# Performance work log

Measured on AMD Instinct MI355X. Metric: run time of the kernel, lower is better.

## Reference

```python
import jax, jax.numpy as jnp
import numpy as np

EPS = 1e-8        # LinearGELU eps
LN_EPS = 1e-5     # LayerNorm eps
NUM_HEADS = 16
DIM = 1024
HIDDEN = 4096
B, N = 4, 785


def _lin(x, xj, w, lw, b=None, lb=None):
    # LinearLinear: primal linear + JVP wrt input and tangent params (lw, lb)
    y = x @ w.T
    yj = xj @ w.T + x @ lw.T
    if b is not None:
        y = y + b
    if lb is not None:
        yj = yj + lb
    return y, yj


def _ln(x, xj, w, b, lw, lb):
    # LinearLayerNorm forward + manual JVP (matches torch source exactly)
    mean = x.mean(-1, keepdims=True)
    xc = x - mean
    var = (xc * xc).mean(-1, keepdims=True)
    std = jnp.sqrt(var + LN_EPS)
    xhat = xc / std
    out = xhat * w + b
    t1 = xhat * lw + lb                              # tangent wrt affine params
    mj = xj.mean(-1, keepdims=True)
    xjc = xj - mj
    a = xjc * std
    corr = 2.0 * (xc * xjc).mean(-1, keepdims=True)
    bterm = (0.5 / std) * corr * xc
    c = (1.0 / std) ** 2 * (a - bterm)
    return out, t1 + c * w


def _gelu(x, xj):
    # exact (erf) GELU; jvp uses gelu(x)/(x+EPS) + x*pdf(x) as in source
    out = 0.5 * x * (1.0 + jax.lax.erf(x * np.float32(1.0 / np.sqrt(2.0))))
    pdf = jnp.exp(-0.5 * x * x) * np.float32(1.0 / np.sqrt(2.0 * np.pi))
    return out, xj * (out / (x + EPS) + x * pdf)


def _attn(x, xj, qkv_w, qkv_lw, proj_w, proj_b, proj_lw, proj_lb):
    Bb, Nn, C = x.shape
    H = NUM_HEADS
    D = C // H
    scale = np.float32(D) ** -0.5
    qkv, qkv_j = _lin(x, xj, qkv_w, qkv_lw)  # [B,N,3C], qkv_bias=False
    def split(t):
        return t.reshape(Bb, Nn, 3, H, D).transpose(2, 0, 3, 1, 4)
    q, k, v = split(qkv)
    qj, kj, vj = split(qkv_j)
    q = q * scale
    qj = qj * scale
    attn = jax.nn.softmax(jnp.einsum('bhnd,bhmd->bhnm', q, k), axis=-1)
    out = jnp.einsum('bhnm,bhmd->bhnd', attn, v)
    # softmax JVP: dm = A_jvp + B_jvp; filter = dm*attn - rowsum(dm*attn)*attn
    dm = jnp.einsum('bhnd,bhmd->bhnm', qj, k) + jnp.einsum('bhnd,bhmd->bhnm', q, kj)
    f = dm * attn
    filt = f - f.sum(-1, keepdims=True) * attn  # == diag(dm @ attn^T) * attn correction
    out_j = jnp.einsum('bhnm,bhmd->bhnd', filt, v) + jnp.einsum('bhnm,bhmd->bhnd', attn, vj)
    out = out.transpose(0, 2, 1, 3).reshape(Bb, Nn, C)
    out_j = out_j.transpose(0, 2, 1, 3).reshape(Bb, Nn, C)
    return _lin(out, out_j, proj_w, proj_lw, proj_b, proj_lb)


def setup_inputs() -> dict:
    keys = jax.random.split(jax.random.key(0), 32)
    ki = iter(keys)
    def nrm(shape, s=0.02):
        return (jax.random.normal(next(ki), shape, jnp.float32) * s).astype(jnp.float32)
    d, h = DIM, HIDDEN
    inp = {
        'input': jax.random.normal(next(ki), (B, N, d), jnp.float32),
        'input_jvp': jax.random.normal(next(ki), (B, N, d), jnp.float32),
        'n1_w': 1.0 + nrm((d,), 0.1), 'n1_b': nrm((d,), 0.1),
        'n1_lw': nrm((d,), 0.1), 'n1_lb': nrm((d,), 0.1),
        'qkv_w': nrm((3 * d, d)), 'qkv_lw': nrm((3 * d, d)),
        'proj_w': nrm((d, d)), 'proj_b': nrm((d,), 0.1),
        'proj_lw': nrm((d, d)), 'proj_lb': nrm((d,), 0.1),
        'n2_w': 1.0 + nrm((d,), 0.1), 'n2_b': nrm((d,), 0.1),
        'n2_lw': nrm((d,), 0.1), 'n2_lb': nrm((d,), 0.1),
        'fc1_w': nrm((h, d)), 'fc1_b': nrm((h,), 0.1),
        'fc1_lw': nrm((h, d)), 'fc1_lb': nrm((h,), 0.1),
        'fc2_w': nrm((d, h)), 'fc2_b': nrm((d,), 0.1),
        'fc2_lw': nrm((d, h)), 'fc2_lb': nrm((d,), 0.1),
    }
    return inp


def reference(input, input_jvp, n1_w, n1_b, n1_lw, n1_lb, qkv_w, qkv_lw,
              proj_w, proj_b, proj_lw, proj_lb, n2_w, n2_b, n2_lw, n2_lb,
              fc1_w, fc1_b, fc1_lw, fc1_lb, fc2_w, fc2_b, fc2_lw, fc2_lb):
    x, xj = _ln(input, input_jvp, n1_w, n1_b, n1_lw, n1_lb)
    x, xj = _attn(x, xj, qkv_w, qkv_lw, proj_w, proj_b, proj_lw, proj_lb)
    x = x + input
    xj = xj + input_jvp
    i2, i2j = x, xj
    x, xj = _ln(x, xj, n2_w, n2_b, n2_lw, n2_lb)
    x, xj = _lin(x, xj, fc1_w, fc1_lw, fc1_b, fc1_lb)
    x, xj = _gelu(x, xj)
    x, xj = _lin(x, xj, fc2_w, fc2_lw, fc2_b, fc2_lb)
    return (x + i2, xj + i2j)
```

## Files before the change

### kernel.cpp

```cpp
#include <hip/hip_runtime.h>
#include <hip/hip_bf16.h>

typedef unsigned short u16;
typedef unsigned int   u32;

#define MP     3328
#define MREAL  3140
#define DIMC   1024
#define H3C    3072
#define HIDC   4096
#define NKV    785
#define SLEN   896

typedef __bf16 bf16x8 __attribute__((ext_vector_type(8)));
typedef float  f32x4  __attribute__((ext_vector_type(4)));

#define MFMA(d,a,b) (d) = __builtin_amdgcn_mfma_f32_16x16x32_bf16((a),(b),(d),0,0,0)

__device__ __forceinline__ u16 f2bf(float f){
  u32 u = __builtin_bit_cast(u32, f);
  return (u16)((u + 0x7fffu + ((u >> 16) & 1u)) >> 16);
}
__device__ __forceinline__ float bf2f(u16 h){
  return __builtin_bit_cast(float, (u32)h << 16);
}
__device__ __forceinline__ void gload16(const u16* g, u16* l){
  __builtin_amdgcn_global_load_lds(
      (const __attribute__((address_space(1))) void*)g,
      (__attribute__((address_space(3))) void*)l, 16, 0, 0);
}
__device__ __forceinline__ float wsum(float v){
  #pragma unroll
  for (int o = 32; o >= 1; o >>= 1) v += __shfl_xor(v, o);
  return v;
}

__global__ __launch_bounds__(256) void cvt_k(const float* __restrict__ in,
                                             u16* __restrict__ out, int n){
  int i = (blockIdx.x * 256 + threadIdx.x) * 4;
  if (i >= n) return;
  float4 v = *(const float4*)(in + i);
  ushort4 o4;
  o4.x = f2bf(v.x); o4.y = f2bf(v.y); o4.z = f2bf(v.z); o4.w = f2bf(v.w);
  *(ushort4*)(out + i) = o4;
}

__global__ __launch_bounds__(256) void ln_jvp_k(
    const float* __restrict__ x, const float* __restrict__ xj,
    const float* __restrict__ w, const float* __restrict__ b,
    const float* __restrict__ lw, const float* __restrict__ lb,
    u16* __restrict__ out, u16* __restrict__ outj)
{
  const int row = blockIdx.x, t = threadIdx.x;
  const size_t ro = (size_t)row * DIMC;
  if (row >= MREAL){
    for (int i = t; i < DIMC; i += 256){ out[ro+i] = 0; outj[ro+i] = 0; }
    return;
  }
  const float4 v  = ((const float4*)(x  + ro))[t];
  const float4 vj = ((const float4*)(xj + ro))[t];
  float sx  = v.x+v.y+v.z+v.w;
  float sxx = v.x*v.x+v.y*v.y+v.z*v.z+v.w*v.w;
  float sj  = vj.x+vj.y+vj.z+vj.w;
  float sxj = v.x*vj.x+v.y*vj.y+v.z*vj.z+v.w*vj.w;
  __shared__ __attribute__((aligned(64))) float red[4][4];
  sx = wsum(sx); sxx = wsum(sxx); sj = wsum(sj); sxj = wsum(sxj);
  const int wid = t>>6, lane = t&63;
  if (lane == 0){ red[wid][0]=sx; red[wid][1]=sxx; red[wid][2]=sj; red[wid][3]=sxj; }
  __syncthreads();
  sx  = red[0][0]+red[1][0]+red[2][0]+red[3][0];
  sxx = red[0][1]+red[1][1]+red[2][1]+red[3][1];
  sj  = red[0][2]+red[1][2]+red[2][2]+red[3][2];
  sxj = red[0][3]+red[1][3]+red[2][3]+red[3][3];
  const float inv  = 1.0f/1024.0f;
  const float mean = sx*inv, meanj = sj*inv;
  const float var  = sxx*inv - mean*mean;
  const float cov  = sxj*inv - mean*meanj;
  const float rstd = rsqrtf(var + 1e-5f);
  const float r3   = rstd*rstd*rstd;
  const float4 wv  = ((const float4*)w)[t];
  const float4 bv  = ((const float4*)b)[t];
  const float4 lwv = ((const float4*)lw)[t];
  const float4 lbv = ((const float4*)lb)[t];
  const float xs[4]  = {v.x,v.y,v.z,v.w},   xjs[4] = {vj.x,vj.y,vj.z,vj.w};
  const float wss[4] = {wv.x,wv.y,wv.z,wv.w}, bs[4] = {bv.x,bv.y,bv.z,bv.w};
  const float lws[4] = {lwv.x,lwv.y,lwv.z,lwv.w}, lbs[4] = {lbv.x,lbv.y,lbv.z,lbv.w};
  const int i0 = t*4;
  #pragma unroll
  for (int e = 0; e < 4; e++){
    const float xc = xs[e]-mean, xjc = xjs[e]-meanj;
    const float xhat = xc*rstd;
    const float cc = xjc*rstd - xc*cov*r3;
    out [ro+i0+e] = f2bf(xhat*wss[e] + bs[e]);
    outj[ro+i0+e] = f2bf(xhat*lws[e] + lbs[e] + cc*wss[e]);
  }
}

template<int EPI>
__global__ __launch_bounds__(512, 1) void gemm_jvp_wide_k(
    const u16* __restrict__ A, const u16* __restrict__ Aj, int lda,
    const u16* __restrict__ B, const u16* __restrict__ Bj, int K,
    const float* __restrict__ bias, const float* __restrict__ biasj,
    void* __restrict__ Yv, void* __restrict__ Yjv, int ldy)
{
  __shared__ __attribute__((aligned(128))) u16 lds[3][24576];
  const int tid = threadIdx.x, wid = tid>>6, lane = tid&63;
  const int l4 = lane>>4, l15 = lane&15;
  const int m0 = blockIdx.y*256, n0 = blockIdx.x*128;
  f32x4 accY[4][4], accJ[4][4];
  #pragma unroll
  for (int i = 0; i < 4; i++)
    #pragma unroll
    for (int j = 0; j < 4; j++){
      accY[i][j] = (f32x4){0.f,0.f,0.f,0.f};
      accJ[i][j] = (f32x4){0.f,0.f,0.f,0.f};
    }
  const int boA0 = tid*16,        boA1 = (512+tid)*16;
  const int sbA0 = boA0 ^ (((boA0>>7)&7)<<4);
  const int sbA1 = boA1 ^ (((boA1>>7)&7)<<4);
  const int rA0 = sbA0>>6, cA0 = (sbA0&63)>>1;
  const int rA1 = sbA1>>6, cA1 = (sbA1&63)>>1;
  const int boB = tid*16;
  const int sbB = boB ^ (((boB>>7)&7)<<4);
  const int rB = sbB>>6, cB = (sbB&63)>>1;
  const u16* srcA0  = A  + (size_t)(m0+rA0)*lda + cA0;
  const u16* srcA1  = A  + (size_t)(m0+rA1)*lda + cA1;
  const u16* srcAj0 = Aj + (size_t)(m0+rA0)*lda + cA0;
  const u16* srcAj1 = Aj + (size_t)(m0+rA1)*lda + cA1;
  const u16* srcB   = B  + (size_t)(n0+rB)*K + cB;
  const u16* srcBj  = Bj + (size_t)(n0+rB)*K + cB;
  const int dA0 = tid*8, dA1 = (512+tid)*8, dB = tid*8;
  const int wr = wid>>1, wc = wid&1;
  int aoff[4], boff[4];
  #pragma unroll
  for (int i = 0; i < 4; i++){
    int ab_ = (wr*64 + i*16 + l15)*64 + l4*16;
    aoff[i] = ab_ ^ (((ab_>>7)&7)<<4);
    int bb_ = (wc*64 + i*16 + l15)*64 + l4*16;
    boff[i] = bb_ ^ (((bb_>>7)&7)<<4);
  }
  auto STAGE = [&](int buf, int t){
    const int k0 = t<<5;
    u16* Lb = &lds[buf][0];
    gload16(srcA0 +k0, Lb + dA0);
    gload16(srcA1 +k0, Lb + dA1);
    gload16(srcAj0+k0, Lb + 8192 + dA0);
    gload16(srcAj1+k0, Lb + 8192 + dA1);
    gload16(srcB  +k0, Lb + 16384 + dB);
    gload16(srcBj +k0, Lb + 20480 + dB);
  };
  const int nt = K >> 5;
  STAGE(0, 0);
  STAGE(1, 1);
  for (int t = 0; t < nt; t++){
    if (t + 1 < nt) asm volatile("s_waitcnt vmcnt(6)" ::: "memory");
    else            asm volatile("s_waitcnt vmcnt(0)" ::: "memory");
    __builtin_amdgcn_s_barrier();
    if (t + 2 < nt) STAGE((t+2)%3, t+2);
    const char* Lb = (const char*)&lds[t%3][0];
    bf16x8 af[4], ajf[4], bbf[4], bjf[4];
    #pragma unroll
    for (int i = 0; i < 4; i++){
      af[i]  = *(const bf16x8*)(Lb + aoff[i]);
      ajf[i] = *(const bf16x8*)(Lb + 16384 + aoff[i]);
      bbf[i] = *(const bf16x8*)(Lb + 32768 + boff[i]);
      bjf[i] = *(const bf16x8*)(Lb + 40960 + boff[i]);
    }
    __builtin_amdgcn_s_setprio(1);
    #pragma unroll
    for (int i = 0; i < 4; i++)
      #pragma unroll
      for (int j = 0; j < 4; j++){
        MFMA(accY[i][j], af[i],  bbf[j]);
        MFMA(accJ[i][j], ajf[i], bbf[j]);
        MFMA(accJ[i][j], af[i],  bjf[j]);
      }
    __builtin_amdgcn_s_setprio(0);
  }
  const int mb = m0 + wr*64 + (l4<<2);
  const int nb = n0 + wc*64 + l15;
  #pragma unroll
  for (int i = 0; i < 4; i++)
    #pragma unroll
    for (int j = 0; j < 4; j++)
      #pragma unroll
      for (int r = 0; r < 4; r++){
        const int m = mb + i*16 + r, n = nb + j*16;
        float y = accY[i][j][r], yj = accJ[i][j][r];
        if (EPI == 0){
          ((u16*)Yv )[(size_t)m*ldy+n] = f2bf(y);
          ((u16*)Yjv)[(size_t)m*ldy+n] = f2bf(yj);
        } else {
          y  += bias[n];
          yj += biasj[n];
          const float ge  = 0.5f*y*(1.0f + erff(y*0.70710678118654752f));
          const float pdf = __expf(-0.5f*y*y)*0.3989422804014327f;
          const float gj  = yj*(ge/(y + 1e-8f) + y*pdf);
          ((u16*)Yv )[(size_t)m*ldy+n] = f2bf(ge);
          ((u16*)Yjv)[(size_t)m*ldy+n] = f2bf(gj);
        }
      }
}

template<int EPI>
__global__ __launch_bounds__(256) void gemm_jvp_k(
    const u16* __restrict__ A, const u16* __restrict__ Aj, int lda,
    const u16* __restrict__ B, const u16* __restrict__ Bj, int K,
    const float* __restrict__ bias, const float* __restrict__ biasj,
    const float* __restrict__ res, const float* __restrict__ resj,
    void* __restrict__ Yv, void* __restrict__ Yjv, int ldy, int mwrite)
{
  __shared__ __attribute__((aligned(128))) u16 lds[3][4][128*32];
  const int tid = threadIdx.x, wid = tid>>6, lane = tid&63;
  const int m0 = blockIdx.y*128, n0 = blockIdx.x*128;
  f32x4 accY[4][4], accJ[4][4];
  #pragma unroll
  for (int i = 0; i < 4; i++)
    #pragma unroll
    for (int j = 0; j < 4; j++){
      accY[i][j] = (f32x4){0.f,0.f,0.f,0.f};
      accJ[i][j] = (f32x4){0.f,0.f,0.f,0.f};
    }
  const int bo0 = wid*1024 + lane*16;
  const int bo1 = bo0 + 4096;
  const int sb0 = bo0 ^ (((bo0>>7)&7)<<4);
  const int sb1 = bo1 ^ (((bo1>>7)&7)<<4);
  const int r0 = sb0>>6, c0 = (sb0&63)>>1;
  const int r1 = sb1>>6, c1 = (sb1&63)>>1;
  const u16* A0  = A  + (size_t)(m0+r0)*lda + c0;
  const u16* A1  = A  + (size_t)(m0+r1)*lda + c1;
  const u16* Aj0 = Aj + (size_t)(m0+r0)*lda + c0;
  const u16* Aj1 = Aj + (size_t)(m0+r1)*lda + c1;
  const u16* B0  = B  + (size_t)(n0+r0)*K + c0;
  const u16* B1  = B  + (size_t)(n0+r1)*K + c1;
  const u16* Bj0 = Bj + (size_t)(n0+r0)*K + c0;
  const u16* Bj1 = Bj + (size_t)(n0+r1)*K + c1;
  const int kq = (lane>>4)<<3;
  const int ar = (wid>>1)*64 + (lane&15);
  const int bc = (wid&1)*64 + (lane&15);
  int aoff[4], boff[4];
  #pragma unroll
  for (int i = 0; i < 4; i++){
    int ab_ = (ar+i*16)*64 + (kq<<1);
    aoff[i] = ab_ ^ (((ab_>>7)&7)<<4);
    int bb_ = (bc+i*16)*64 + (kq<<1);
    boff[i] = bb_ ^ (((bb_>>7)&7)<<4);
  }
  auto STAGE = [&](int buf, int t){
    const int k0 = t<<5;
    u16* p0 = &lds[buf][0][0];
    gload16(A0 +k0, p0+(bo0>>1)); gload16(A1 +k0, p0+(bo1>>1));
    u16* p1 = &lds[buf][1][0];
    gload16(Aj0+k0, p1+(bo0>>1)); gload16(Aj1+k0, p1+(bo1>>1));
    u16* p2 = &lds[buf][2][0];
    gload16(B0 +k0, p2+(bo0>>1)); gload16(B1 +k0, p2+(bo1>>1));
    u16* p3 = &lds[buf][3][0];
    gload16(Bj0+k0, p3+(bo0>>1)); gload16(Bj1+k0, p3+(bo1>>1));
  };
  const int nt = K >> 5;
  STAGE(0, 0);
  STAGE(1, 1);
  for (int t = 0; t < nt; t++){
    if (t + 1 < nt) asm volatile("s_waitcnt vmcnt(8)" ::: "memory");
    else            asm volatile("s_waitcnt vmcnt(0)" ::: "memory");
    __builtin_amdgcn_s_barrier();
    if (t + 2 < nt) STAGE((t+2)%3, t+2);
    const char* lAb  = (const char*)&lds[t%3][0][0];
    const char* lAjb = (const char*)&lds[t%3][1][0];
    const char* lBb  = (const char*)&lds[t%3][2][0];
    const char* lBjb = (const char*)&lds[t%3][3][0];
    bf16x8 af[4], ajf[4], bbf[4], bjf[4];
    #pragma unroll
    for (int i = 0; i < 4; i++){
      af[i]  = *(const bf16x8*)(lAb  + aoff[i]);
      ajf[i] = *(const bf16x8*)(lAjb + aoff[i]);
      bbf[i] = *(const bf16x8*)(lBb  + boff[i]);
      bjf[i] = *(const bf16x8*)(lBjb + boff[i]);
    }
    __builtin_amdgcn_s_setprio(1);
    #pragma unroll
    for (int i = 0; i < 4; i++)
      #pragma unroll
      for (int j = 0; j < 4; j++){
        MFMA(accY[i][j], af[i],  bbf[j]);
        MFMA(accJ[i][j], ajf[i], bbf[j]);
        MFMA(accJ[i][j], af[i],  bjf[j]);
      }
    __builtin_amdgcn_s_setprio(0);
  }
  const int mb = m0 + (wid>>1)*64 + ((lane>>4)<<2);
  const int nb = n0 + (wid&1)*64 + (lane&15);
  #pragma unroll
  for (int i = 0; i < 4; i++)
    #pragma unroll
    for (int j = 0; j < 4; j++)
      #pragma unroll
      for (int r = 0; r < 4; r++){
        const int m = mb + i*16 + r, n = nb + j*16;
        float y = accY[i][j][r], yj = accJ[i][j][r];
        if (EPI == 0){
          ((u16*)Yv )[(size_t)m*ldy+n] = f2bf(y);
          ((u16*)Yjv)[(size_t)m*ldy+n] = f2bf(yj);
        } else if (EPI == 1){
          if (m < mwrite){
            y  += bias[n]  + res [(size_t)m*ldy+n];
            yj += biasj[n] + resj[(size_t)m*ldy+n];
            ((float*)Yv )[(size_t)m*ldy+n] = y;
            ((float*)Yjv)[(size_t)m*ldy+n] = yj;
          }
        } else {
          y  += bias[n];
          yj += biasj[n];
          const float ge  = 0.5f*y*(1.0f + erff(y*0.70710678118654752f));
          const float pdf = __expf(-0.5f*y*y)*0.3989422804014327f;
          const float gj  = yj*(ge/(y + 1e-8f) + y*pdf);
          ((u16*)Yv )[(size_t)m*ldy+n] = f2bf(ge);
          ((u16*)Yjv)[(size_t)m*ldy+n] = f2bf(gj);
        }
      }
}

__global__ __launch_bounds__(256) void transpose_v_k(
    const u16* __restrict__ qkvb, const u16* __restrict__ qkvjb,
    u16* __restrict__ vT, u16* __restrict__ vjT)
{
  __shared__ __attribute__((aligned(64))) u16 tl[64][80];
  __shared__ __attribute__((aligned(64))) u16 tlj[64][80];
  const int kt = blockIdx.x, bh = blockIdx.y;
  const int b = bh>>4, h = bh&15;
  const int t = threadIdx.x;
  const int kv = t>>2, dd = (t&3)*16;
  const int kvg = kt*64 + kv;
  if (kvg < NKV){
    const u16* s0 = qkvb  + (size_t)(b*NKV+kvg)*H3C + 2048 + h*64 + dd;
    const u16* s1 = qkvjb + (size_t)(b*NKV+kvg)*H3C + 2048 + h*64 + dd;
    *(uint4*)&tl [kv][dd]   = *(const uint4*)s0;
    *(uint4*)&tl [kv][dd+8] = *(const uint4*)(s0+8);
    *(uint4*)&tlj[kv][dd]   = *(const uint4*)s1;
    *(uint4*)&tlj[kv][dd+8] = *(const uint4*)(s1+8);
  } else {
    uint4 z = {0,0,0,0};
    *(uint4*)&tl [kv][dd] = z; *(uint4*)&tl [kv][dd+8] = z;
    *(uint4*)&tlj[kv][dd] = z; *(uint4*)&tlj[kv][dd+8] = z;
  }
  __syncthreads();
  const int d = t>>2, kc = (t&3)*16;
  u16* d0 = vT  + ((size_t)bh*64 + d)*SLEN + kt*64 + kc;
  u16* d1 = vjT + ((size_t)bh*64 + d)*SLEN + kt*64 + kc;
  #pragma unroll
  for (int e = 0; e < 16; e++){ d0[e] = tl[kc+e][d]; d1[e] = tlj[kc+e][d]; }
}

__global__ __launch_bounds__(256) void flash_attn_jvp_k(
    const u16* __restrict__ qkvb, const u16* __restrict__ qkvjb,
    const u16* __restrict__ vT, const u16* __restrict__ vjT,
    u16* __restrict__ o, u16* __restrict__ oj)
{
  __shared__ __attribute__((aligned(64))) u16 lK  [64*64];
  __shared__ __attribute__((aligned(64))) u16 lKj [64*64];
  __shared__ __attribute__((aligned(64))) u16 lvT [64*64];
  __shared__ __attribute__((aligned(64))) u16 lvjT[64*64];
  __shared__ __attribute__((aligned(64))) u16 pl  [128*64];
  __shared__ __attribute__((aligned(64))) u16 pdl [128*64];
  const int tid = threadIdx.x, wid = tid>>6, lane = tid&63;
  const int l4 = lane>>4, l15 = lane&15;
  const int qt = blockIdx.x, bh = blockIdx.y, b = bh>>4, h = bh&15;

  bf16x8 qf[2][2], qjf[2][2];
  {
    const size_t qrb = (size_t)b*NKV + qt*128 + wid*32;
    #pragma unroll
    for (int i = 0; i < 2; i++){
      const size_t ro = (qrb + i*16 + l15)*H3C + h*64;
      #pragma unroll
      for (int ks = 0; ks < 2; ks++){
        qf [i][ks] = *(const bf16x8*)(qkvb  + ro + ks*32 + l4*8);
        qjf[i][ks] = *(const bf16x8*)(qkvjb + ro + ks*32 + l4*8);
      }
    }
  }
  float m_st[2][4], l_st[2][4], g_st[2][4];
  f32x4 PO[2][4], PTJ[2][4];
  #pragma unroll
  for (int i = 0; i < 2; i++)
    #pragma unroll
    for (int r = 0; r < 4; r++){
      m_st[i][r] = -1e30f; l_st[i][r] = 0.f; g_st[i][r] = 0.f;
    }
  #pragma unroll
  for (int i = 0; i < 2; i++)
    #pragma unroll
    for (int j = 0; j < 4; j++){
      PO[i][j] = (f32x4){0.f,0.f,0.f,0.f};
      PTJ[i][j] = (f32x4){0.f,0.f,0.f,0.f};
    }
  const char* lKb   = (const char*)lK;
  const char* lKjb  = (const char*)lKj;
  const char* lvTb  = (const char*)lvT;
  const char* lvjTb = (const char*)lvjT;
  char* plb  = (char*)pl;
  char* pdlb = (char*)pdl;

  for (int t = 0; t < 13; t++){
    #pragma unroll
    for (int rnd = 0; rnd < 2; rnd++){
      const int gidx = rnd*256 + tid;
      const int row = gidx>>3, c = gidx&7;
      const int cs = c ^ (row&7);
      const size_t ksrc = (size_t)(b*NKV + t*64 + row)*H3C + 1024 + h*64 + cs*8;
      gload16(qkvb  + ksrc, lK  + gidx*8);
      gload16(qkvjb + ksrc, lKj + gidx*8);
      const size_t vsrc = ((size_t)bh*64 + row)*SLEN + t*64 + cs*8;
      gload16(vT  + vsrc, lvT  + gidx*8);
      gload16(vjT + vsrc, lvjT + gidx*8);
    }
    __syncthreads();

    #pragma unroll
    for (int i = 0; i < 2; i++){
      f32x4 s[4], dm[4];
      #pragma unroll
      for (int j = 0; j < 4; j++){
        s[j] = (f32x4){0.f,0.f,0.f,0.f};
        dm[j] = (f32x4){0.f,0.f,0.f,0.f};
      }
      #pragma unroll
      for (int ks = 0; ks < 2; ks++){
        #pragma unroll
        for (int j = 0; j < 4; j++){
          const int row = j*16 + l15;
          const int byt = (row*128 + ks*64 + l4*16) ^ ((row&7)<<4);
          const bf16x8 kf  = *(const bf16x8*)(lKb  + byt);
          const bf16x8 kjf = *(const bf16x8*)(lKjb + byt);
          MFMA(s[j],  qf[i][ks],  kf);
          MFMA(dm[j], qjf[i][ks], kf);
          MFMA(dm[j], qf[i][ks],  kjf);
        }
      }
      float tm[4] = {-1e30f,-1e30f,-1e30f,-1e30f};
      #pragma unroll
      for (int j = 0; j < 4; j++){
        const int colg = t*64 + j*16 + l15;
        #pragma unroll
        for (int r = 0; r < 4; r++){
          float sv = s[j][r]*0.125f;
          if (colg >= NKV) sv = -1e30f;
          s[j][r] = sv;
          dm[j][r] *= 0.125f;
          tm[r] = fmaxf(tm[r], sv);
        }
      }
      #pragma unroll
      for (int r = 0; r < 4; r++){
        float v = tm[r];
        v = fmaxf(v, __shfl_xor(v, 1));
        v = fmaxf(v, __shfl_xor(v, 2));
        v = fmaxf(v, __shfl_xor(v, 4));
        v = fmaxf(v, __shfl_xor(v, 8));
        const float mn = fmaxf(m_st[i][r], v);
        const float sc = __expf(m_st[i][r] - mn);
        m_st[i][r] = mn;
        l_st[i][r] *= sc;
        g_st[i][r] *= sc;
        #pragma unroll
        for (int j = 0; j < 4; j++){ PO[i][j][r] *= sc; PTJ[i][j][r] *= sc; }
      }
      float ps[4] = {0.f,0.f,0.f,0.f}, pds[4] = {0.f,0.f,0.f,0.f};
      #pragma unroll
      for (int j = 0; j < 4; j++){
        const int col = j*16 + l15;
        #pragma unroll
        for (int r = 0; r < 4; r++){
          const float p  = __expf(s[j][r] - m_st[i][r]);
          const float pd = p * dm[j][r];
          ps[r] += p; pds[r] += pd;
          const int row = wid*32 + i*16 + l4*4 + r;
          const int byt = (row*128 + col*2) ^ ((row&7)<<4);
          *(u16*)(plb  + byt) = f2bf(p);
          *(u16*)(pdlb + byt) = f2bf(pd);
        }
      }
      #pragma unroll
      for (int r = 0; r < 4; r++){
        float v = ps[r], w = pds[r];
        v += __shfl_xor(v, 1); w += __shfl_xor(w, 1);
        v += __shfl_xor(v, 2); w += __shfl_xor(w, 2);
        v += __shfl_xor(v, 4); w += __shfl_xor(w, 4);
        v += __shfl_xor(v, 8); w += __shfl_xor(w, 8);
        l_st[i][r] += v; g_st[i][r] += w;
      }
    }

    #pragma unroll
    for (int ks = 0; ks < 2; ks++){
      bf16x8 pa[2], pda[2];
      #pragma unroll
      for (int i = 0; i < 2; i++){
        const int row = wid*32 + i*16 + l15;
        const int byt = (row*128 + ks*64 + l4*16) ^ ((row&7)<<4);
        pa[i]  = *(const bf16x8*)(plb  + byt);
        pda[i] = *(const bf16x8*)(pdlb + byt);
      }
      #pragma unroll
      for (int j = 0; j < 4; j++){
        const int row = j*16 + l15;
        const int byt = (row*128 + ks*64 + l4*16) ^ ((row&7)<<4);
        const bf16x8 vb  = *(const bf16x8*)(lvTb  + byt);
        const bf16x8 vjb = *(const bf16x8*)(lvjTb + byt);
        #pragma unroll
        for (int i = 0; i < 2; i++){
          MFMA(PO[i][j],  pa[i],  vb);
          MFMA(PTJ[i][j], pda[i], vb);
          MFMA(PTJ[i][j], pa[i],  vjb);
        }
      }
    }
    __syncthreads();
  }

  #pragma unroll
  for (int i = 0; i < 2; i++)
    #pragma unroll
    for (int r = 0; r < 4; r++){
      const int ql = qt*128 + wid*32 + i*16 + l4*4 + r;
      if (ql < NKV){
        const float rl = 1.0f / l_st[i][r];
        const float gg = g_st[i][r] * rl;
        #pragma unroll
        for (int j = 0; j < 4; j++){
          const size_t oo = ((size_t)b*NKV + ql)*DIMC + h*64 + j*16 + l15;
          const float po = PO[i][j][r] * rl;
          o [oo] = f2bf(po);
          oj[oo] = f2bf(PTJ[i][j][r]*rl - gg*po);
        }
      }
    }
}

extern "C" void kernel_launch(void* const* d_in, const int* in_sizes, int n_in,
                              void* d_out, int out_size, void* d_ws, size_t ws_size,
                              hipStream_t stream)
{
  (void)in_sizes; (void)n_in; (void)out_size;
  const float* input   = (const float*)d_in[0];
  const float* inputj  = (const float*)d_in[1];
  const float* n1_w    = (const float*)d_in[2];
  const float* n1_b    = (const float*)d_in[3];
  const float* n1_lw   = (const float*)d_in[4];
  const float* n1_lb   = (const float*)d_in[5];
  const float* qkv_w   = (const float*)d_in[6];
  const float* qkv_lw  = (const float*)d_in[7];
  const float* proj_w  = (const float*)d_in[8];
  const float* proj_b  = (const float*)d_in[9];
  const float* proj_lw = (const float*)d_in[10];
  const float* proj_lb = (const float*)d_in[11];
  const float* n2_w    = (const float*)d_in[12];
  const float* n2_b    = (const float*)d_in[13];
  const float* n2_lw   = (const float*)d_in[14];
  const float* n2_lb   = (const float*)d_in[15];
  const float* fc1_w   = (const float*)d_in[16];
  const float* fc1_b   = (const float*)d_in[17];
  const float* fc1_lw  = (const float*)d_in[18];
  const float* fc1_lb  = (const float*)d_in[19];
  const float* fc2_w   = (const float*)d_in[20];
  const float* fc2_b   = (const float*)d_in[21];
  const float* fc2_lw  = (const float*)d_in[22];
  const float* fc2_lb  = (const float*)d_in[23];

  const size_t SZ_W      = 2u*4194304u*2u;
  const size_t SZ_ARENA1 = 2u*(size_t)MP*HIDC*2u;
  const size_t SZ_VT     = (size_t)64*64*SLEN*2u;
  const size_t SZ_ARENA2 = 2u*SZ_VT;
  const size_t SZ_ARENA3 = 2u*(size_t)MP*DIMC*2u;
  const size_t SZ_X2     = (size_t)MP*DIMC*4u;
  const size_t NEEDED = SZ_W + SZ_ARENA1 + SZ_ARENA2 + SZ_ARENA3 + 2u*SZ_X2 + 4096u;
  if (ws_size < NEEDED) return;

  char* base = (char*)d_ws;
  size_t off = 0;
  auto ab = [&](size_t bytes)->char*{
    char* p = base + off;
    off += bytes; off = (off + 255) & ~(size_t)255;
    return p;
  };
  char* Wslot  = ab(SZ_W);
  char* arena1 = ab(SZ_ARENA1);
  char* arena2 = ab(SZ_ARENA2);
  char* arena3 = ab(SZ_ARENA3);
  float* x2  = (float*)ab(SZ_X2);
  float* x2j = (float*)ab(SZ_X2);

  u16* wbuf  = (u16*)Wslot;
  u16* wjbuf = wbuf + 4194304;
  u16* qkvb  = (u16*)arena1;
  u16* qkvjb = qkvb + (size_t)MP*H3C;
  u16* hb    = (u16*)arena1;
  u16* hjb   = hb + (size_t)MP*HIDC;
  u16* vT    = (u16*)arena2;
  u16* vjT   = vT + (size_t)64*64*SLEN;
  u16* x3b   = (u16*)arena2;
  u16* x3jb  = x3b + (size_t)MP*DIMC;
  u16* x1b   = (u16*)arena3;
  u16* x1jb  = x1b + (size_t)MP*DIMC;
  u16* ob    = (u16*)arena3;
  u16* ojb   = ob + (size_t)MP*DIMC;

  auto cvt = [&](const float* src, u16* dst, int n){
    cvt_k<<<dim3((n + 1023)/1024), 256, 0, stream>>>(src, dst, n);
  };

  ln_jvp_k<<<dim3(MP), 256, 0, stream>>>(input, inputj, n1_w, n1_b, n1_lw, n1_lb,
                                         x1b, x1jb);
  cvt(qkv_w, wbuf, H3C*DIMC); cvt(qkv_lw, wjbuf, H3C*DIMC);
  gemm_jvp_wide_k<0><<<dim3(H3C/128, MP/256), 512, 0, stream>>>(
      x1b, x1jb, DIMC, wbuf, wjbuf, DIMC, nullptr, nullptr,
      qkvb, qkvjb, H3C);
  transpose_v_k<<<dim3(14, 64), 256, 0, stream>>>(qkvb, qkvjb, vT, vjT);
  flash_attn_jvp_k<<<dim3(7, 64), 256, 0, stream>>>(qkvb, qkvjb, vT, vjT, ob, ojb);
  cvt(proj_w, wbuf, DIMC*DIMC); cvt(proj_lw, wjbuf, DIMC*DIMC);
  gemm_jvp_k<1><<<dim3(DIMC/128, MP/128), 256, 0, stream>>>(
      ob, ojb, DIMC, wbuf, wjbuf, DIMC, proj_b, proj_lb, input, inputj,
      x2, x2j, DIMC, MREAL);
  ln_jvp_k<<<dim3(MP), 256, 0, stream>>>(x2, x2j, n2_w, n2_b, n2_lw, n2_lb,
                                         x3b, x3jb);
  cvt(fc1_w, wbuf, HIDC*DIMC); cvt(fc1_lw, wjbuf, HIDC*DIMC);
  gemm_jvp_wide_k<2><<<dim3(HIDC/128, MP/256), 512, 0, stream>>>(
      x3b, x3jb, DIMC, wbuf, wjbuf, DIMC, fc1_b, fc1_lb,
      hb, hjb, HIDC);
  cvt(fc2_w, wbuf, DIMC*HIDC); cvt(fc2_lw, wjbuf, DIMC*HIDC);
  float* out0 = (float*)d_out;
  float* out1 = out0 + (size_t)MREAL*DIMC;
  gemm_jvp_k<1><<<dim3(DIMC/128, MP/128), 256, 0, stream>>>(
      hb, hjb, HIDC, wbuf, wjbuf, HIDC, fc2_b, fc2_lb, x2, x2j,
      out0, out1, DIMC, MREAL);
}
```

Baseline: 557.2 us.

## Retile wide JVP GEMM to 128x256 with 4 waves, XCD-aware block remap, fused cvt

The wide GEMM used for QKV and FC1 changes from 512 threads with 256x128 tiles to 256 threads with 128x256 tiles. Each wave now holds a 64x128 output with 4x8 accumulator pairs, so every A fragment loaded from LDS is reused across twice as many MFMAs. Both GEMM kernels remap block indices round-robin over 8 chiplets so that neighbouring tiles land on the same XCD and share L2. The two weight-conversion launches per layer are merged into one kernel. The costs are much higher register pressure (256 fp32 accumulator values per lane) and fewer, larger blocks per GEMM.

```diff
diff --git a/kernel.cpp b/kernel.cpp
--- a/kernel.cpp
+++ b/kernel.cpp
@@ -35,14 +35,18 @@
   return v;
 }
 
-__global__ __launch_bounds__(256) void cvt_k(const float* __restrict__ in,
-                                             u16* __restrict__ out, int n){
+__global__ __launch_bounds__(256) void cvt2_k(
+    const float* __restrict__ in0, u16* __restrict__ out0, int n0,
+    const float* __restrict__ in1, u16* __restrict__ out1, int n1)
+{
   int i = (blockIdx.x * 256 + threadIdx.x) * 4;
-  if (i >= n) return;
-  float4 v = *(const float4*)(in + i);
+  const float* src; u16* dst;
+  if (i < n0){ src = in0 + i; dst = out0 + i; }
+  else { int j = i - n0; if (j >= n1) return; src = in1 + j; dst = out1 + j; }
+  float4 v = *(const float4*)src;
   ushort4 o4;
   o4.x = f2bf(v.x); o4.y = f2bf(v.y); o4.z = f2bf(v.z); o4.w = f2bf(v.w);
-  *(ushort4*)(out + i) = o4;
+  *(ushort4*)dst = o4;
 }
 
 __global__ __launch_bounds__(256) void ln_jvp_k(
@@ -97,7 +101,7 @@
 }
 
 template<int EPI>
-__global__ __launch_bounds__(512, 1) void gemm_jvp_wide_k(
+__global__ __launch_bounds__(256, 1) void gemm_jvp_v2_k(
     const u16* __restrict__ A, const u16* __restrict__ Aj, int lda,
     const u16* __restrict__ B, const u16* __restrict__ Bj, int K,
     const float* __restrict__ bias, const float* __restrict__ biasj,
@@ -106,71 +110,96 @@
   __shared__ __attribute__((aligned(128))) u16 lds[3][24576];
   const int tid = threadIdx.x, wid = tid>>6, lane = tid&63;
   const int l4 = lane>>4, l15 = lane&15;
-  const int m0 = blockIdx.y*256, n0 = blockIdx.x*128;
-  f32x4 accY[4][4], accJ[4][4];
+  const int ord = blockIdx.y * gridDim.x + blockIdx.x;
+  const int cpx = (gridDim.x * gridDim.y) >> 3;
+  const int nb  = (ord & 7) * cpx + (ord >> 3);
+  const int m0 = (nb / gridDim.x) * 128;
+  const int n0 = (nb % gridDim.x) * 256;
+  f32x4 accY[4][8], accJ[4][8];
   #pragma unroll
   for (int i = 0; i < 4; i++)
     #pragma unroll
-    for (int j = 0; j < 4; j++){
+    for (int j = 0; j < 8; j++){
       accY[i][j] = (f32x4){0.f,0.f,0.f,0.f};
       accJ[i][j] = (f32x4){0.f,0.f,0.f,0.f};
     }
-  const int boA0 = tid*16,        boA1 = (512+tid)*16;
-  const int sbA0 = boA0 ^ (((boA0>>7)&7)<<4);
-  const int sbA1 = boA1 ^ (((boA1>>7)&7)<<4);
-  const int rA0 = sbA0>>6, cA0 = (sbA0&63)>>1;
-  const int rA1 = sbA1>>6, cA1 = (sbA1&63)>>1;
-  const int boB = tid*16;
-  const int sbB = boB ^ (((boB>>7)&7)<<4);
-  const int rB = sbB>>6, cB = (sbB&63)>>1;
+  const int bA0 = tid*16,        bA1 = (256+tid)*16;
+  const int sA0 = bA0 ^ (((bA0>>7)&7)<<4), sA1 = bA1 ^ (((bA1>>7)&7)<<4);
+  const int rA0 = sA0>>6, cA0 = (sA0&63)>>1;
+  const int rA1 = sA1>>6, cA1 = (sA1&63)>>1;
+  int rB[4], cB[4];
+  #pragma unroll
+  for (int g = 0; g < 4; g++){
+    const int bb = (g*256 + tid)*16;
+    const int sb = bb ^ (((bb>>7)&7)<<4);
+    rB[g] = sb>>6; cB[g] = (sb&63)>>1;
+  }
   const u16* srcA0  = A  + (size_t)(m0+rA0)*lda + cA0;
   const u16* srcA1  = A  + (size_t)(m0+rA1)*lda + cA1;
   const u16* srcAj0 = Aj + (size_t)(m0+rA0)*lda + cA0;
   const u16* srcAj1 = Aj + (size_t)(m0+rA1)*lda + cA1;
-  const u16* srcB   = B  + (size_t)(n0+rB)*K + cB;
-  const u16* srcBj  = Bj + (size_t)(n0+rB)*K + cB;
-  const int dA0 = tid*8, dA1 = (512+tid)*8, dB = tid*8;
+  const u16* srcB0  = B  + (size_t)(n0+rB[0])*K + cB[0];
+  const u16* srcB1  = B  + (size_t)(n0+rB[1])*K + cB[1];
+  const u16* srcB2  = B  + (size_t)(n0+rB[2])*K + cB[2];
+  const u16* srcB3  = B  + (size_t)(n0+rB[3])*K + cB[3];
+  const u16* srcBj0 = Bj + (size_t)(n0+rB[0])*K + cB[0];
+  const u16* srcBj1 = Bj + (size_t)(n0+rB[1])*K + cB[1];
+  const u16* srcBj2 = Bj + (size_t)(n0+rB[2])*K + cB[2];
+  const u16* srcBj3 = Bj + (size_t)(n0+rB[3])*K + cB[3];
+  const int dA0 = tid*8, dA1 = (256+tid)*8;
   const int wr = wid>>1, wc = wid&1;
-  int aoff[4], boff[4];
+  int aoff[4], boff[8];
   #pragma unroll
   for (int i = 0; i < 4; i++){
     int ab_ = (wr*64 + i*16 + l15)*64 + l4*16;
     aoff[i] = ab_ ^ (((ab_>>7)&7)<<4);
-    int bb_ = (wc*64 + i*16 + l15)*64 + l4*16;
-    boff[i] = bb_ ^ (((bb_>>7)&7)<<4);
+  }
+  #pragma unroll
+  for (int j = 0; j < 8; j++){
+    int bb_ = (wc*128 + j*16 + l15)*64 + l4*16;
+    boff[j] = bb_ ^ (((bb_>>7)&7)<<4);
   }
   auto STAGE = [&](int buf, int t){
     const int k0 = t<<5;
     u16* Lb = &lds[buf][0];
     gload16(srcA0 +k0, Lb + dA0);
     gload16(srcA1 +k0, Lb + dA1);
-    gload16(srcAj0+k0, Lb + 8192 + dA0);
-    gload16(srcAj1+k0, Lb + 8192 + dA1);
-    gload16(srcB  +k0, Lb + 16384 + dB);
-    gload16(srcBj +k0, Lb + 20480 + dB);
+    gload16(srcAj0+k0, Lb + 4096 + dA0);
+    gload16(srcAj1+k0, Lb + 4096 + dA1);
+    gload16(srcB0 +k0, Lb + 8192  + tid*8);
+    gload16(srcB1 +k0, Lb + 8192  + (256+tid)*8);
+    gload16(srcB2 +k0, Lb + 8192  + (512+tid)*8);
+    gload16(srcB3 +k0, Lb + 8192  + (768+tid)*8);
+    gload16(srcBj0+k0, Lb + 16384 + tid*8);
+    gload16(srcBj1+k0, Lb + 16384 + (256+tid)*8);
+    gload16(srcBj2+k0, Lb + 16384 + (512+tid)*8);
+    gload16(srcBj3+k0, Lb + 16384 + (768+tid)*8);
   };
   const int nt = K >> 5;
   STAGE(0, 0);
   STAGE(1, 1);
   for (int t = 0; t < nt; t++){
-    if (t + 1 < nt) asm volatile("s_waitcnt vmcnt(6)" ::: "memory");
+    if (t + 1 < nt) asm volatile("s_waitcnt vmcnt(12)" ::: "memory");
     else            asm volatile("s_waitcnt vmcnt(0)" ::: "memory");
     __builtin_amdgcn_s_barrier();
     if (t + 2 < nt) STAGE((t+2)%3, t+2);
     const char* Lb = (const char*)&lds[t%3][0];
-    bf16x8 af[4], ajf[4], bbf[4], bjf[4];
+    bf16x8 af[4], ajf[4], bbf[8], bjf[8];
     #pragma unroll
     for (int i = 0; i < 4; i++){
       af[i]  = *(const bf16x8*)(Lb + aoff[i]);
-      ajf[i] = *(const bf16x8*)(Lb + 16384 + aoff[i]);
-      bbf[i] = *(const bf16x8*)(Lb + 32768 + boff[i]);
-      bjf[i] = *(const bf16x8*)(Lb + 40960 + boff[i]);
+      ajf[i] = *(const bf16x8*)(Lb + 8192 + aoff[i]);
+    }
+    #pragma unroll
+    for (int j = 0; j < 8; j++){
+      bbf[j] = *(const bf16x8*)(Lb + 16384 + boff[j]);
+      bjf[j] = *(const bf16x8*)(Lb + 32768 + boff[j]);
     }
     __builtin_amdgcn_s_setprio(1);
     #pragma unroll
     for (int i = 0; i < 4; i++)
       #pragma unroll
-      for (int j = 0; j < 4; j++){
+      for (int j = 0; j < 8; j++){
         MFMA(accY[i][j], af[i],  bbf[j]);
         MFMA(accJ[i][j], ajf[i], bbf[j]);
         MFMA(accJ[i][j], af[i],  bjf[j]);
@@ -178,14 +207,14 @@
     __builtin_amdgcn_s_setprio(0);
   }
   const int mb = m0 + wr*64 + (l4<<2);
-  const int nb = n0 + wc*64 + l15;
+  const int nbase = n0 + wc*128 + l15;
   #pragma unroll
   for (int i = 0; i < 4; i++)
     #pragma unroll
-    for (int j = 0; j < 4; j++)
+    for (int j = 0; j < 8; j++)
       #pragma unroll
       for (int r = 0; r < 4; r++){
-        const int m = mb + i*16 + r, n = nb + j*16;
+        const int m = mb + i*16 + r, n = nbase + j*16;
         float y = accY[i][j][r], yj = accJ[i][j][r];
         if (EPI == 0){
           ((u16*)Yv )[(size_t)m*ldy+n] = f2bf(y);
@@ -212,7 +241,11 @@
 {
   __shared__ __attribute__((aligned(128))) u16 lds[3][4][128*32];
   const int tid = threadIdx.x, wid = tid>>6, lane = tid&63;
-  const int m0 = blockIdx.y*128, n0 = blockIdx.x*128;
+  const int ord = blockIdx.y * gridDim.x + blockIdx.x;
+  const int cpx = (gridDim.x * gridDim.y) >> 3;
+  const int nbk = (ord & 7) * cpx + (ord >> 3);
+  const int m0 = (nbk / gridDim.x) * 128;
+  const int n0 = (nbk % gridDim.x) * 128;
   f32x4 accY[4][4], accJ[4][4];
   #pragma unroll
   for (int i = 0; i < 4; i++)
@@ -605,29 +638,30 @@
   u16* ob    = (u16*)arena3;
   u16* ojb   = ob + (size_t)MP*DIMC;
 
-  auto cvt = [&](const float* src, u16* dst, int n){
-    cvt_k<<<dim3((n + 1023)/1024), 256, 0, stream>>>(src, dst, n);
+  auto cvt2 = [&](const float* s0, u16* d0, int n0,
+                  const float* s1, u16* d1, int n1){
+    cvt2_k<<<dim3((n0 + n1 + 1023)/1024), 256, 0, stream>>>(s0, d0, n0, s1, d1, n1);
   };
 
   ln_jvp_k<<<dim3(MP), 256, 0, stream>>>(input, inputj, n1_w, n1_b, n1_lw, n1_lb,
                                          x1b, x1jb);
-  cvt(qkv_w, wbuf, H3C*DIMC); cvt(qkv_lw, wjbuf, H3C*DIMC);
-  gemm_jvp_wide_k<0><<<dim3(H3C/128, MP/256), 512, 0, stream>>>(
+  cvt2(qkv_w, wbuf, H3C*DIMC, qkv_lw, wjbuf, H3C*DIMC);
+  gemm_jvp_v2_k<0><<<dim3(H3C/256, MP/128), 256, 0, stream>>>(
       x1b, x1jb, DIMC, wbuf, wjbuf, DIMC, nullptr, nullptr,
       qkvb, qkvjb, H3C);
   transpose_v_k<<<dim3(14, 64), 256, 0, stream>>>(qkvb, qkvjb, vT, vjT);
   flash_attn_jvp_k<<<dim3(7, 64), 256, 0, stream>>>(qkvb, qkvjb, vT, vjT, ob, ojb);
-  cvt(proj_w, wbuf, DIMC*DIMC); cvt(proj_lw, wjbuf, DIMC*DIMC);
+  cvt2(proj_w, wbuf, DIMC*DIMC, proj_lw, wjbuf, DIMC*DIMC);
   gemm_jvp_k<1><<<dim3(DIMC/128, MP/128), 256, 0, stream>>>(
       ob, ojb, DIMC, wbuf, wjbuf, DIMC, proj_b, proj_lb, input, inputj,
       x2, x2j, DIMC, MREAL);
   ln_jvp_k<<<dim3(MP), 256, 0, stream>>>(x2, x2j, n2_w, n2_b, n2_lw, n2_lb,
                                          x3b, x3jb);
-  cvt(fc1_w, wbuf, HIDC*DIMC); cvt(fc1_lw, wjbuf, HIDC*DIMC);
-  gemm_jvp_wide_k<2><<<dim3(HIDC/128, MP/256), 512, 0, stream>>>(
+  cvt2(fc1_w, wbuf, HIDC*DIMC, fc1_lw, wjbuf, HIDC*DIMC);
+  gemm_jvp_v2_k<2><<<dim3(HIDC/256, MP/128), 256, 0, stream>>>(
       x3b, x3jb, DIMC, wbuf, wjbuf, DIMC, fc1_b, fc1_lb,
       hb, hjb, HIDC);
-  cvt(fc2_w, wbuf, DIMC*HIDC); cvt(fc2_lw, wjbuf, DIMC*HIDC);
+  cvt2(fc2_w, wbuf, DIMC*HIDC, fc2_lw, wjbuf, DIMC*HIDC);
   float* out0 = (float*)d_out;
   float* out1 = out0 + (size_t)MREAL*DIMC;
   gemm_jvp_k<1><<<dim3(DIMC/128, MP/128), 256, 0, stream>>>(
```

Result: slower. 599.0 us (+7.5%).
